# Optimization experiments

Measured on AMD Instinct MI355X. Metric: run time of the kernel, lower is better.

Reference implementation:

```python
import jax, jax.numpy as jnp
import numpy as np

M_RANGE = 5
K = 2 * M_RANGE + 1      # 11
N_CLASS = K * K          # 121
IM_CHANNEL = 3


def _gconv(x, w, groups):
    # torch F.conv2d(x, w, None, stride=1, padding=M_RANGE, dilation=1, groups)
    return jax.lax.conv_general_dilated(
        x, w, window_strides=(1, 1),
        padding=[(M_RANGE, M_RANGE)] * 2,
        dimension_numbers=('NCHW', 'OIHW', 'NCHW'),
        feature_group_count=groups)


def setup_inputs() -> dict:
    key = jax.random.key(0)
    k1, k2 = jax.random.split(key)
    B, H, W = 8, 128, 128
    im_input = jax.random.normal(k1, (B, 2 * IM_CHANNEL, H, W), jnp.float32)
    # motion in [-m_range, m_range-1) so idx and idx+1 stay in [0, K-1]
    gt_motion = jax.random.uniform(k2, (B, 2, H, W), jnp.float32,
                                   minval=-float(M_RANGE), maxval=float(M_RANGE - 1) - 1e-3)
    # canonical one-hot displacement kernels, [n_class, 1, K, K] (torch OIHW after swapaxes)
    m_kernel = jnp.eye(N_CLASS, dtype=jnp.float32).reshape(N_CLASS, 1, K, K)
    return {"im_input": im_input, "gt_motion": gt_motion, "m_kernel": m_kernel}


def motion2mask(motion):
    # vectorized version of the per-pixel bilinear one-hot construction
    mf = jnp.floor(motion)
    frac = motion - mf                              # [B,2,H,W]
    idx = mf.astype(jnp.int32) + M_RANGE            # [B,2,H,W]
    grid = jnp.arange(K)[None, :, None, None]       # [1,K,1,1]

    def onehot(i, f):                               # i,f: [B,H,W] -> [B,K,H,W]
        i = i[:, None]
        f = f[:, None]
        return jnp.where(grid == i, 1.0 - f, 0.0) + jnp.where(grid == i + 1, f, 0.0)

    a = onehot(idx[:, 0], frac[:, 0])               # x-axis weights
    b = onehot(idx[:, 1], frac[:, 1])               # y-axis weights
    B, _, H, W = motion.shape
    # torch.ger(b, a).view(-1): channel = by*K + ax
    return (b[:, :, None] * a[:, None, :]).reshape(B, N_CLASS, H, W)


def reference(im_input, gt_motion, m_kernel):
    B, _, H, W = gt_motion.shape
    m_mask = motion2mask(gt_motion)                          # [B,C,H,W]
    out_mask = _gconv(m_mask, m_kernel, N_CLASS)             # [B,C,H,W]
    # construct_seg
    ones = jnp.ones_like(out_mask)
    seg = (_gconv(ones, m_kernel, N_CLASS) * out_mask).sum(1)  # [B,H,W]
    appear = jax.nn.relu(1.0 - seg)
    disappear = jax.nn.relu(seg - 1.0)
    # construct_image
    im = im_input[:, -IM_CHANNEL:] * (1.0 - disappear)[:, None]   # [B,ch,H,W]
    im_exp = jnp.repeat(im, N_CLASS, axis=1)                      # [B,ch*C,H,W]
    w_tiled = jnp.tile(m_kernel, (IM_CHANNEL, 1, 1, 1))           # [ch*C,1,K,K]
    nearby = _gconv(im_exp, w_tiled, IM_CHANNEL * N_CLASS)
    nearby = nearby.reshape(B, IM_CHANNEL, N_CLASS, H, W)
    pred = (nearby * out_mask[:, None]).sum(2)                    # [B,ch,H,W]
    return pred, m_mask, disappear, appear
```

## Files before the change

### kernel.cpp

```cpp
#include <hip/hip_runtime.h>

#define HW       16384
#define NCLASS   121

#define OFF_PRED 0
#define OFF_MASK (8 * 3 * HW)
#define OFF_DIS  (OFF_MASK + 8 * NCLASS * HW)
#define OFF_APP  (OFF_DIS + 8 * HW)

#define NSEGBLK  256
#define NPREDBLK 768
#define NMASKBLK (8 * 16 * 11)

#define SENT 100000.0f

typedef float nfloat4 __attribute__((ext_vector_type(4)));

__device__ __forceinline__ float hatf(float u) { return fmaxf(0.f, 1.f - fabsf(u)); }

__device__ __forceinline__ void nt_store4(float* p, float a, float b, float c, float d) {
    nfloat4 nv; nv.x = a; nv.y = b; nv.z = c; nv.w = d;
    __builtin_nontemporal_store(nv, (nfloat4*)p);
}

__global__ __launch_bounds__(256) void k_seg(const float* __restrict__ motion,
                                             float* __restrict__ out) {
    __shared__ float sseg[4 * 128];
    int blk = blockIdx.x;
    int b   = blk >> 5;
    int y0  = (blk & 31) << 2;
    int tid = threadIdx.x;

    const float* motx = motion + (size_t)(b * 2) * HW;
    const float* moty = motx + HW;

    float mxv[7], myv[7];
    #pragma unroll
    for (int it = 0; it < 7; ++it) {
        int idx = tid + it * 256;
        int sy  = y0 - 5 + (idx >> 7);
        int sx  = idx & 127;
        bool ok = (sy >= 0) && (sy < 128);
        int s   = (ok ? sy : 0) * 128 + sx;
        float mx = motx[s];
        float my = moty[s];
        mxv[it] = ok ? mx : SENT;
        myv[it] = ok ? my : SENT;
    }
    asm volatile("" ::: "memory");

    ((float2*)sseg)[tid] = make_float2(0.f, 0.f);
    __syncthreads();

    #pragma unroll
    for (int it = 0; it < 7; ++it) {
        int idx = tid + it * 256;
        int sy  = y0 - 5 + (idx >> 7);
        int sx  = idx & 127;
        float mx = mxv[it], my = myv[it];
        float flx = floorf(mx), fly = floorf(my);
        float fa = mx - flx, fb = my - fly;
        int ia = (int)flx + 5, ib = (int)fly + 5;
        float wa0 = 1.f - fa, wa1 = fa;
        float wb0 = 1.f - fb, wb1 = fb;
        #pragma unroll
        for (int j = 0; j < 2; ++j) {
            int ty = sy - (ib + j) + 5;
            if (ty < y0 || ty >= y0 + 4) continue;
            float wb = j ? wb1 : wb0;
            #pragma unroll
            for (int i = 0; i < 2; ++i) {
                int tx = sx - (ia + i) + 5;
                if (tx < 0 || tx >= 128) continue;
                atomicAdd(&sseg[(ty - y0) * 128 + tx], wb * (i ? wa1 : wa0));
            }
        }
    }
    __syncthreads();

    int p2 = tid * 2;
    int ly = p2 >> 7;
    int x  = p2 & 127;
    float2 s2 = *(float2*)&sseg[ly * 128 + x];
    float2 d2, a2;
    d2.x = fmaxf(s2.x - 1.f, 0.f); a2.x = fmaxf(1.f - s2.x, 0.f);
    d2.y = fmaxf(s2.y - 1.f, 0.f); a2.y = fmaxf(1.f - s2.y, 0.f);
    int p = b * HW + (y0 + ly) * 128 + x;
    *(float2*)(out + OFF_DIS + p) = d2;
    *(float2*)(out + OFF_APP + p) = a2;
}

__global__ __launch_bounds__(256) void k_maskpred(const float* __restrict__ motion,
                                                  const float* __restrict__ im_input,
                                                  float* __restrict__ out) {
    __shared__ float spred[4 * 128];
    int tid = threadIdx.x;
    int blk = blockIdx.x;

    if (blk < NPREDBLK) {
        int c  = blk >> 8;
        int t  = blk & 255;
        int b  = t >> 5;
        int y0 = (t & 31) << 2;
        const float* motx = motion + (size_t)(b * 2) * HW;
        const float* moty = motx + HW;
        const float* imc  = im_input + (size_t)(b * 6 + 3 + c) * HW;
        const float* disb = out + OFF_DIS + (size_t)b * HW;

        float mxv[7], myv[7], imv[7], dsv[7];
        #pragma unroll
        for (int it = 0; it < 7; ++it) {
            int idx = tid + it * 256;
            int sy  = y0 - 5 + (idx >> 7);
            int sx  = idx & 127;
            bool ok = (sy >= 0) && (sy < 128);
            int s   = (ok ? sy : 0) * 128 + sx;
            float mx = motx[s];
            float my = moty[s];
            float im = imc[s];
            float ds = disb[s];
            mxv[it] = ok ? mx : SENT;
            myv[it] = ok ? my : SENT;
            imv[it] = ok ? im : 0.f;
            dsv[it] = ds;
        }
        asm volatile("" ::: "memory");

        ((float2*)spred)[tid] = make_float2(0.f, 0.f);
        __syncthreads();

        #pragma unroll
        for (int it = 0; it < 7; ++it) {
            int idx = tid + it * 256;
            int sy  = y0 - 5 + (idx >> 7);
            int sx  = idx & 127;
            float mx = mxv[it], my = myv[it];
            float iv = imv[it] * (1.f - dsv[it]);
            float flx = floorf(mx), fly = floorf(my);
            float fa = mx - flx, fb = my - fly;
            int ia = (int)flx + 5, ib = (int)fly + 5;
            float wa0 = 1.f - fa, wa1 = fa;
            float wb0 = 1.f - fb, wb1 = fb;
            #pragma unroll
            for (int j = 0; j < 2; ++j) {
                int ty = sy - (ib + j) + 5;
                if (ty < y0 || ty >= y0 + 4) continue;
                float wb = j ? wb1 : wb0;
                #pragma unroll
                for (int i = 0; i < 2; ++i) {
                    int tx = sx - (ia + i) + 5;
                    if (tx < 0 || tx >= 128) continue;
                    atomicAdd(&spred[(ty - y0) * 128 + tx], wb * (i ? wa1 : wa0) * iv);
                }
            }
        }
        __syncthreads();

        int p2 = tid * 2;
        int ly = p2 >> 7;
        int x  = p2 & 127;
        float2 v = *(float2*)&spred[ly * 128 + x];
        float* predb = out + OFF_PRED + (size_t)(b * 3 + c) * HW + (y0 + ly) * 128 + x;
        *(float2*)predb = v;
    } else {
        int mb = blk - NPREDBLK;
        int kb = mb % 11;
        int tl = mb / 11;
        int b  = tl >> 4;
        int y0 = (tl & 15) << 3;
        const float* motx = motion + (size_t)(b * 2) * HW;
        const float* moty = motx + HW;

        int ly = tid >> 5;
        int x4 = (tid & 31) << 2;
        int g  = (y0 + ly) * 128 + x4;
        float4 mx = *(const float4*)(motx + g);
        float4 my = *(const float4*)(moty + g);
        float kbo = (float)(kb - 5);
        float4 bv;
        bv.x = hatf(my.x - kbo); bv.y = hatf(my.y - kbo);
        bv.z = hatf(my.z - kbo); bv.w = hatf(my.w - kbo);
        float* mm = out + OFF_MASK + ((size_t)(b * NCLASS + kb * 11)) * HW + g;
        #pragma unroll
        for (int ka = 0; ka < 11; ++ka) {
            float kao = (float)(ka - 5);
            nt_store4(mm + (size_t)ka * HW,
                      bv.x * hatf(mx.x - kao),
                      bv.y * hatf(mx.y - kao),
                      bv.z * hatf(mx.z - kao),
                      bv.w * hatf(mx.w - kao));
        }
    }
}

extern "C" void kernel_launch(void* const* d_in, const int* in_sizes, int n_in,
                              void* d_out, int out_size, void* d_ws, size_t ws_size,
                              hipStream_t stream) {
    const float* im_input = (const float*)d_in[0];
    const float* motion   = (const float*)d_in[1];
    float* out = (float*)d_out;

    k_seg<<<dim3(NSEGBLK), dim3(256), 0, stream>>>(motion, out);
    k_maskpred<<<dim3(NPREDBLK + NMASKBLK), dim3(256), 0, stream>>>(motion, im_input, out);
}
```

Measured before the change: 21.65 us.

## Retile seg kernel to one row per block and use 512-thread maskpred blocks

The seg kernel now assigns one output row per block (1024 blocks) with float4 loads of the 11-row halo, instead of four rows per block, which raises parallelism but increases redundant halo reads. The maskpred kernel moves to 512-thread blocks: pred blocks keep the 4-row tile but use fewer loop iterations per thread, and mask blocks cover 16 rows each. These changes aim to improve occupancy and latency hiding in the small seg kernel and to cut per-thread work in pred, at the cost of more global reads of motion data.

New measurement: 21.93 us. Within noise of the previous version (+1.3%).

```diff
diff --git a/kernel.cpp b/kernel.cpp
--- a/kernel.cpp
+++ b/kernel.cpp
@@ -8,9 +8,8 @@
 #define OFF_DIS  (OFF_MASK + 8 * NCLASS * HW)
 #define OFF_APP  (OFF_DIS + 8 * HW)
 
-#define NSEGBLK  256
 #define NPREDBLK 768
-#define NMASKBLK (8 * 16 * 11)
+#define NMASKBLK (8 * 8 * 11)
 
 #define SENT 100000.0f
 
@@ -25,72 +24,75 @@
 
 __global__ __launch_bounds__(256) void k_seg(const float* __restrict__ motion,
                                              float* __restrict__ out) {
-    __shared__ float sseg[4 * 128];
+    __shared__ float sseg[128];
+    int tid = threadIdx.x;
     int blk = blockIdx.x;
-    int b   = blk >> 5;
-    int y0  = (blk & 31) << 2;
-    int tid = threadIdx.x;
+    int b   = blk >> 7;
+    int y0  = blk & 127;
 
     const float* motx = motion + (size_t)(b * 2) * HW;
     const float* moty = motx + HW;
 
-    float mxv[7], myv[7];
+    float4 mx4[2], my4[2];
+    int syv[2], sxv[2];
     #pragma unroll
-    for (int it = 0; it < 7; ++it) {
-        int idx = tid + it * 256;
-        int sy  = y0 - 5 + (idx >> 7);
-        int sx  = idx & 127;
-        bool ok = (sy >= 0) && (sy < 128);
-        int s   = (ok ? sy : 0) * 128 + sx;
-        float mx = motx[s];
-        float my = moty[s];
-        mxv[it] = ok ? mx : SENT;
-        myv[it] = ok ? my : SENT;
-    }
-    asm volatile("" ::: "memory");
-
-    ((float2*)sseg)[tid] = make_float2(0.f, 0.f);
+    for (int g = 0; g < 2; ++g) {
+        int idx4 = g * 256 + tid;
+        int r    = idx4 >> 5;
+        int sx   = (idx4 & 31) << 2;
+        int sy   = y0 - 5 + r;
+        bool ok  = (idx4 < 352) && (sy >= 0) && (sy < 128);
+        int s    = (ok ? sy : 0) * 128 + sx;
+        float4 a = *(const float4*)(motx + s);
+        float4 c = *(const float4*)(moty + s);
+        float4 sn = make_float4(SENT, SENT, SENT, SENT);
+        mx4[g] = ok ? a : sn;
+        my4[g] = ok ? c : sn;
+        syv[g] = sy; sxv[g] = sx;
+    }
+
+    if (tid < 128) sseg[tid] = 0.f;
     __syncthreads();
 
     #pragma unroll
-    for (int it = 0; it < 7; ++it) {
-        int idx = tid + it * 256;
-        int sy  = y0 - 5 + (idx >> 7);
-        int sx  = idx & 127;
-        float mx = mxv[it], my = myv[it];
-        float flx = floorf(mx), fly = floorf(my);
-        float fa = mx - flx, fb = my - fly;
-        int ia = (int)flx + 5, ib = (int)fly + 5;
-        float wa0 = 1.f - fa, wa1 = fa;
-        float wb0 = 1.f - fb, wb1 = fb;
-        #pragma unroll
-        for (int j = 0; j < 2; ++j) {
-            int ty = sy - (ib + j) + 5;
-            if (ty < y0 || ty >= y0 + 4) continue;
-            float wb = j ? wb1 : wb0;
+    for (int g = 0; g < 2; ++g) {
+        const float* mxp = (const float*)&mx4[g];
+        const float* myp = (const float*)&my4[g];
+        int sy = syv[g];
+        #pragma unroll
+        for (int p = 0; p < 4; ++p) {
+            float mx = mxp[p], my = myp[p];
+            int sx = sxv[g] + p;
+            float flx = floorf(mx), fly = floorf(my);
+            float fa = mx - flx, fb = my - fly;
+            int ia = (int)flx + 5, ib = (int)fly + 5;
+            float wa0 = 1.f - fa, wa1 = fa;
+            float wb0 = 1.f - fb, wb1 = fb;
             #pragma unroll
-            for (int i = 0; i < 2; ++i) {
-                int tx = sx - (ia + i) + 5;
-                if (tx < 0 || tx >= 128) continue;
-                atomicAdd(&sseg[(ty - y0) * 128 + tx], wb * (i ? wa1 : wa0));
+            for (int j = 0; j < 2; ++j) {
+                int ty = sy - (ib + j) + 5;
+                if (ty != y0) continue;
+                float wb = j ? wb1 : wb0;
+                #pragma unroll
+                for (int i = 0; i < 2; ++i) {
+                    int tx = sx - (ia + i) + 5;
+                    if (tx < 0 || tx >= 128) continue;
+                    atomicAdd(&sseg[tx], wb * (i ? wa1 : wa0));
+                }
             }
         }
     }
     __syncthreads();
 
-    int p2 = tid * 2;
-    int ly = p2 >> 7;
-    int x  = p2 & 127;
-    float2 s2 = *(float2*)&sseg[ly * 128 + x];
-    float2 d2, a2;
-    d2.x = fmaxf(s2.x - 1.f, 0.f); a2.x = fmaxf(1.f - s2.x, 0.f);
-    d2.y = fmaxf(s2.y - 1.f, 0.f); a2.y = fmaxf(1.f - s2.y, 0.f);
-    int p = b * HW + (y0 + ly) * 128 + x;
-    *(float2*)(out + OFF_DIS + p) = d2;
-    *(float2*)(out + OFF_APP + p) = a2;
-}
-
-__global__ __launch_bounds__(256) void k_maskpred(const float* __restrict__ motion,
+    if (tid < 128) {
+        float v = sseg[tid];
+        int p = b * HW + y0 * 128 + tid;
+        out[OFF_DIS + p] = fmaxf(v - 1.f, 0.f);
+        out[OFF_APP + p] = fmaxf(1.f - v, 0.f);
+    }
+}
+
+__global__ __launch_bounds__(512) void k_maskpred(const float* __restrict__ motion,
                                                   const float* __restrict__ im_input,
                                                   float* __restrict__ out) {
     __shared__ float spred[4 * 128];
@@ -107,13 +109,13 @@
         const float* imc  = im_input + (size_t)(b * 6 + 3 + c) * HW;
         const float* disb = out + OFF_DIS + (size_t)b * HW;
 
-        float mxv[7], myv[7], imv[7], dsv[7];
-        #pragma unroll
-        for (int it = 0; it < 7; ++it) {
-            int idx = tid + it * 256;
+        float mxv[4], myv[4], imv[4], dsv[4];
+        #pragma unroll
+        for (int it = 0; it < 4; ++it) {
+            int idx = tid + it * 512;
             int sy  = y0 - 5 + (idx >> 7);
             int sx  = idx & 127;
-            bool ok = (sy >= 0) && (sy < 128);
+            bool ok = (idx < 1792) && (sy >= 0) && (sy < 128);
             int s   = (ok ? sy : 0) * 128 + sx;
             float mx = motx[s];
             float my = moty[s];
@@ -124,14 +126,13 @@
             imv[it] = ok ? im : 0.f;
             dsv[it] = ds;
         }
-        asm volatile("" ::: "memory");
-
-        ((float2*)spred)[tid] = make_float2(0.f, 0.f);
+
+        spred[tid] = 0.f;
         __syncthreads();
 
         #pragma unroll
-        for (int it = 0; it < 7; ++it) {
-            int idx = tid + it * 256;
+        for (int it = 0; it < 4; ++it) {
+            int idx = tid + it * 512;
             int sy  = y0 - 5 + (idx >> 7);
             int sx  = idx & 127;
             float mx = mxv[it], my = myv[it];
@@ -156,18 +157,15 @@
         }
         __syncthreads();
 
-        int p2 = tid * 2;
-        int ly = p2 >> 7;
-        int x  = p2 & 127;
-        float2 v = *(float2*)&spred[ly * 128 + x];
-        float* predb = out + OFF_PRED + (size_t)(b * 3 + c) * HW + (y0 + ly) * 128 + x;
-        *(float2*)predb = v;
+        int ly = tid >> 7;
+        int x  = tid & 127;
+        out[OFF_PRED + (size_t)(b * 3 + c) * HW + (y0 + ly) * 128 + x] = spred[tid];
     } else {
         int mb = blk - NPREDBLK;
         int kb = mb % 11;
         int tl = mb / 11;
-        int b  = tl >> 4;
-        int y0 = (tl & 15) << 3;
+        int b  = tl >> 3;
+        int y0 = (tl & 7) << 4;
         const float* motx = motion + (size_t)(b * 2) * HW;
         const float* moty = motx + HW;
 
@@ -200,6 +198,6 @@
     const float* motion   = (const float*)d_in[1];
     float* out = (float*)d_out;
 
-    k_seg<<<dim3(NSEGBLK), dim3(256), 0, stream>>>(motion, out);
-    k_maskpred<<<dim3(NPREDBLK + NMASKBLK), dim3(256), 0, stream>>>(motion, im_input, out);
-}
+    k_seg<<<dim3(1024), dim3(256), 0, stream>>>(motion, out);
+    k_maskpred<<<dim3(NPREDBLK + NMASKBLK), dim3(512), 0, stream>>>(motion, im_input, out);
+}
```
